# Performance work log

Hardware: AMD Instinct MI355X
Metric: run time of the kernel (lower is better)

## Reference

```python
import jax, jax.numpy as jnp
import numpy as np

EMB_DIM = 1024
N_HEADS = 16
HEAD_DIM = EMB_DIM // N_HEADS


def setup_inputs() -> dict:
    key = jax.random.key(0)
    ks = jax.random.split(key, 6)
    B, T, C = 2, 2048, EMB_DIM
    s = 1.0 / np.sqrt(C)
    return {
        "x": jax.random.normal(ks[0], (B, T, C), dtype=jnp.float32),
        "W_query": jax.random.normal(ks[1], (C, C), dtype=jnp.float32) * s,
        "W_key": jax.random.normal(ks[2], (C, C), dtype=jnp.float32) * s,
        "W_value": jax.random.normal(ks[3], (C, C), dtype=jnp.float32) * s,
        "W_out": jax.random.normal(ks[4], (C, C), dtype=jnp.float32) * s,
        "b_out": jax.random.normal(ks[5], (C,), dtype=jnp.float32) * 0.01,
    }


def reference(x, W_query, W_key, W_value, W_out, b_out):
    # x: [B, T, C]. Linear weights stored as [in, out] (transposed torch layout).
    B, T, C = x.shape
    H, D = N_HEADS, HEAD_DIM

    def split_heads(t):  # [B,T,C] -> [B,H,T,D]
        return t.reshape(B, T, H, D).transpose(0, 2, 1, 3)

    q = split_heads(x @ W_query)
    k = split_heads(x @ W_key)
    v = split_heads(x @ W_value)

    scale = 1.0 / jnp.sqrt(jnp.asarray(D, dtype=x.dtype))
    att = jnp.einsum("bhqd,bhkd->bhqk", q, k) * scale  # [B,H,T,T]
    causal = jnp.tril(jnp.ones((T, T), dtype=bool))
    att = jnp.where(causal[None, None], att, jnp.asarray(-jnp.inf, dtype=att.dtype))
    att = jax.nn.softmax(att, axis=-1)
    # dropout is identity in eval / drop_rate=0
    y = jnp.einsum("bhqk,bhkd->bhqd", att, v)  # [B,H,T,D]
    y = y.transpose(0, 2, 1, 3).reshape(B, T, C)
    return y @ W_out + b_out
```

## Files before the change

kernel.cpp:

```cpp
#include <hip/hip_runtime.h>
#include <hip/hip_bf16.h>
#include <math.h>

#define Bsz 2
#define Tsz 2048
#define Csz 1024
#define Hsz 16
#define Dsz 64

typedef __attribute__((ext_vector_type(8))) short frag8;
typedef __attribute__((ext_vector_type(4))) float f4;
typedef __attribute__((ext_vector_type(8))) unsigned short us8;
typedef __attribute__((ext_vector_type(4))) _Float16 frag4h;
typedef __attribute__((ext_vector_type(8))) _Float16 frag8h;

static __device__ __forceinline__ unsigned short f2bf(float f) {
  union { __hip_bfloat16 h; unsigned short u; } c;
  c.h = __float2bfloat16(f);
  return c.u;
}
static __device__ __forceinline__ unsigned short f2h(float f) {
  union { _Float16 h; unsigned short u; } c;
  c.h = (_Float16)f;
  return c.u;
}

#define GLDS16(g, l)                                                        \
  __builtin_amdgcn_global_load_lds(                                         \
      (const __attribute__((address_space(1))) void*)(g),                   \
      (__attribute__((address_space(3))) void*)(l), 16, 0, 0)

#define QSCALE 0.18033688f

__global__ __launch_bounds__(256) void cast_x(const float* __restrict__ x,
                                              unsigned short* __restrict__ xb) {
  const int i = (blockIdx.x * 256 + threadIdx.x) * 8;
  const float4 a = *(const float4*)(x + i);
  const float4 b = *(const float4*)(x + i + 4);
  us8 v;
  v[0] = f2bf(a.x); v[1] = f2bf(a.y); v[2] = f2bf(a.z); v[3] = f2bf(a.w);
  v[4] = f2bf(b.x); v[5] = f2bf(b.y); v[6] = f2bf(b.z); v[7] = f2bf(b.w);
  *(us8*)(xb + i) = v;
}

__global__ __launch_bounds__(256) void transpose_cast(
    const float* __restrict__ s0, const float* __restrict__ s1,
    const float* __restrict__ s2, const float* __restrict__ s3,
    unsigned short* __restrict__ d0, unsigned short* __restrict__ d1,
    unsigned short* __restrict__ d2, unsigned short* __restrict__ d3) {
  __shared__ float Ls[64][65];
  const int mat = blockIdx.x >> 8;
  const int tile = blockIdx.x & 255;
  const float* src = mat == 0 ? s0 : mat == 1 ? s1 : mat == 2 ? s2 : s3;
  unsigned short* dst = mat == 0 ? d0 : mat == 1 ? d1 : mat == 2 ? d2 : d3;
  const int tr0 = (tile >> 4) << 6, tc0 = (tile & 15) << 6;
  const int t = threadIdx.x;
  const int lr = t >> 4, lc = (t & 15) << 2;
#pragma unroll
  for (int j = 0; j < 4; ++j) {
    const float4 v = *(const float4*)(src + (size_t)(tr0 + lr + j * 16) * 1024 + tc0 + lc);
    Ls[lr + j * 16][lc + 0] = v.x;
    Ls[lr + j * 16][lc + 1] = v.y;
    Ls[lr + j * 16][lc + 2] = v.z;
    Ls[lr + j * 16][lc + 3] = v.w;
  }
  __syncthreads();
#pragma unroll
  for (int j = 0; j < 4; ++j) {
    ushort4 v;
    v.x = f2bf(Ls[lc + 0][lr + j * 16]);
    v.y = f2bf(Ls[lc + 1][lr + j * 16]);
    v.z = f2bf(Ls[lc + 2][lr + j * 16]);
    v.w = f2bf(Ls[lc + 3][lr + j * 16]);
    *(ushort4*)(dst + (size_t)(tc0 + lr + j * 16) * 1024 + tr0 + lc) = v;
  }
}

template <int MODE, int MT>
__global__ __launch_bounds__(256) void mm_bt(
    const unsigned short* __restrict__ A, const unsigned short* __restrict__ Bt,
    const float* __restrict__ bias, unsigned short* __restrict__ O0,
    unsigned short* __restrict__ O1, unsigned short* __restrict__ O2,
    float* __restrict__ Of) {
  __shared__ __align__(16) unsigned short As[MT * 32 * 64];
  __shared__ __align__(16) unsigned short Bs[128 * 64];
  const int K = 1024;
  const int tid = threadIdx.x;
  const int wave = tid >> 6, lane = tid & 63;
  const int quad = lane >> 4, l16 = lane & 15;
  const int wrow = (wave >> 1) * (MT * 16), wn = wave & 1;
  const int row0 = blockIdx.y * (MT * 32), col0 = blockIdx.x << 7;

  const int sr = lane >> 3, sg = lane & 7;
  const int g0 = sg ^ sr;
  const unsigned short* gA = A + (size_t)(row0 + wave * (MT * 8) + sr) * K + (g0 << 3);
  const unsigned short* gB = Bt + (size_t)(col0 + wave * 32 + sr) * K + (g0 << 3);

  f4 acc[MT][4];
#pragma unroll
  for (int i = 0; i < MT; ++i)
#pragma unroll
    for (int j = 0; j < 4; ++j) acc[i][j] = (f4){0.f, 0.f, 0.f, 0.f};

  for (int kk = 0; kk < K; kk += 64) {
    __syncthreads();
#pragma unroll
    for (int s = 0; s < MT; ++s)
      GLDS16(gA + kk + (size_t)(s * 8) * K, &As[(wave * (MT * 8) + s * 8) * 64]);
#pragma unroll
    for (int s = 0; s < 4; ++s)
      GLDS16(gB + kk + (size_t)(s * 8) * K, &Bs[(wave * 32 + s * 8) * 64]);
    __syncthreads();

#pragma unroll
    for (int ks = 0; ks < 2; ++ks) {
      frag8 af[MT], bf[4];
#pragma unroll
      for (int mt = 0; mt < MT; ++mt) {
        const int r = wrow + mt * 16 + l16;
        af[mt] = *(const frag8*)&As[r * 64 + (((ks * 4 + quad) ^ (l16 & 7)) << 3)];
      }
#pragma unroll
      for (int nt = 0; nt < 4; ++nt) {
        const int n = wn * 64 + nt * 16 + l16;
        bf[nt] = *(const frag8*)&Bs[n * 64 + (((ks * 4 + quad) ^ (l16 & 7)) << 3)];
      }
#pragma unroll
      for (int mt = 0; mt < MT; ++mt)
#pragma unroll
        for (int nt = 0; nt < 4; ++nt)
          acc[mt][nt] = __builtin_amdgcn_mfma_f32_16x16x32_bf16(af[mt], bf[nt], acc[mt][nt], 0, 0, 0);
    }
  }

  if (MODE == 0) {
    if (col0 < 2048) {
      const bool isK = (col0 >= 1024);
      unsigned short* dst = isK ? O1 : O0;
      const float sc = isK ? 1.0f : QSCALE;
#pragma unroll
      for (int mt = 0; mt < MT; ++mt)
#pragma unroll
        for (int nt = 0; nt < 4; ++nt) {
          const int m = row0 + wrow + mt * 16 + quad * 4;
          const int n = (col0 & 1023) + wn * 64 + nt * 16 + l16;
          const int b = m >> 11, h = n >> 6, d = n & 63;
#pragma unroll
          for (int r = 0; r < 4; ++r) {
            const int tk = (m + r) & (Tsz - 1);
            dst[(((size_t)b * Hsz + h) * Tsz + tk) * Dsz + d] = f2bf(acc[mt][nt][r] * sc);
          }
        }
    } else {
#pragma unroll
      for (int mt = 0; mt < MT; ++mt)
#pragma unroll
        for (int nt = 0; nt < 4; ++nt) {
          const int tok = row0 + wrow + mt * 16 + quad * 4;
          const int ch = (col0 - 2048) + wn * 64 + nt * 16 + l16;
          const int b = tok >> 11, tk = tok & (Tsz - 1);
          const int h = ch >> 6, d = ch & 63;
          const int t5 = tk & 31;
          const int pos = (tk & ~31) + ((t5 >> 4) << 2) + (((t5 >> 2) & 3) << 3) + (t5 & 3);
          ushort4 v;
          v.x = f2h(acc[mt][nt][0]); v.y = f2h(acc[mt][nt][1]);
          v.z = f2h(acc[mt][nt][2]); v.w = f2h(acc[mt][nt][3]);
          *(ushort4*)&O2[(((size_t)b * Hsz + h) * Dsz + d) * Tsz + pos] = v;
        }
    }
  } else {
#pragma unroll
    for (int mt = 0; mt < MT; ++mt)
#pragma unroll
      for (int nt = 0; nt < 4; ++nt) {
        const int m = row0 + wrow + mt * 16 + quad * 4;
        const int n = col0 + wn * 64 + nt * 16 + l16;
        const float bv = bias[n];
#pragma unroll
        for (int r = 0; r < 4; ++r)
          Of[(size_t)(m + r) * Csz + n] = acc[mt][nt][r] + bv;
      }
  }
}

__global__ __launch_bounds__(256, 1) void attn_mfma(
    const unsigned short* __restrict__ Qb,
    const unsigned short* __restrict__ Kb,
    const unsigned short* __restrict__ VTb,
    unsigned short* __restrict__ Y) {
  __shared__ __align__(16) unsigned short Ks[2][2048];
  __shared__ __align__(16) unsigned short Vs[2][2048];

  const int tid = threadIdx.x;
  const int wave = tid >> 6, lane = tid & 63;
  const int quad = lane >> 4, l16 = lane & 15;

  const int bh = blockIdx.x & 31;
  const int jg = blockIdx.x >> 5;
  const int ja = 4 * jg + wave;
  const int jb = 63 - ja;
  const int qa = ja << 5, qb = jb << 5;

  const unsigned short* Qh = Qb + (size_t)bh * Tsz * Dsz;
  const unsigned short* Kh = Kb + (size_t)bh * Tsz * Dsz;
  const unsigned short* Vh = VTb + (size_t)bh * Dsz * Tsz;

  const int kkey = tid >> 3, kc = tid & 7;
  const int vd = tid >> 2, vc = tid & 3;
  const unsigned short* gK = Kh + (size_t)kkey * Dsz + ((kc ^ (kkey & 7)) << 3);
  const unsigned short* gV = Vh + (size_t)vd * Tsz + ((vc ^ ((vd + (vd >> 2)) & 3)) << 3);

  frag8 qfa[2][2], qfb[2][2];
#pragma unroll
  for (int m = 0; m < 2; ++m)
#pragma unroll
    for (int ks = 0; ks < 2; ++ks) {
      qfa[m][ks] = *(const frag8*)(Qh + (size_t)(qa + m * 16 + l16) * Dsz + ks * 32 + quad * 8);
      qfb[m][ks] = *(const frag8*)(Qh + (size_t)(qb + m * 16 + l16) * Dsz + ks * 32 + quad * 8);
    }

  f4 oa[2][4], ob[2][4];
  float lsa[2] = {0.f, 0.f}, lsb[2] = {0.f, 0.f};
#pragma unroll
  for (int m = 0; m < 2; ++m)
#pragma unroll
    for (int nt = 0; nt < 4; ++nt) {
      oa[m][nt] = (f4){0.f, 0.f, 0.f, 0.f};
      ob[m][nt] = (f4){0.f, 0.f, 0.f, 0.f};
    }
  const f4 zf = (f4){0.f, 0.f, 0.f, 0.f};
  const int fl = (l16 + (l16 >> 2)) & 3;

  const int nch = 64 - 4 * jg;

  GLDS16(gK, &Ks[0][wave * 512]);
  GLDS16(gV, &Vs[0][wave * 512]);
  GLDS16(gK + (size_t)32 * Dsz, &Ks[1][wave * 512]);
  GLDS16(gV + 32, &Vs[1][wave * 512]);
  __syncthreads();

  for (int i = 0; i < nch; ++i) {
    const int bsel = i & 1;
    if (i <= jb) {
      frag8 kf[2][2];
#pragma unroll
      for (int n = 0; n < 2; ++n)
#pragma unroll
        for (int ks = 0; ks < 2; ++ks)
          kf[n][ks] = *(const frag8*)&Ks[bsel][(n * 16 + l16) * 64 + (((ks * 4 + quad) ^ (l16 & 7)) << 3)];
      frag8h vf[4];
#pragma unroll
      for (int nt = 0; nt < 4; ++nt)
        vf[nt] = *(const frag8h*)&Vs[bsel][(nt * 16 + l16) * 32 + ((quad ^ fl) << 3)];

      {
        f4 st[2][2];
#pragma unroll
        for (int n = 0; n < 2; ++n)
#pragma unroll
          for (int m = 0; m < 2; ++m) {
            f4 a = __builtin_amdgcn_mfma_f32_16x16x32_bf16(kf[n][0], qfb[m][0], zf, 0, 0, 0);
            st[n][m] = __builtin_amdgcn_mfma_f32_16x16x32_bf16(kf[n][1], qfb[m][1], a, 0, 0, 0);
          }
        const bool dm = (i == jb);
        frag4h paf[2][2];
#pragma unroll
        for (int m = 0; m < 2; ++m) {
          const int qq = m * 16 + l16;
#pragma unroll
          for (int n = 0; n < 2; ++n) {
            const int key0 = n * 16 + quad * 4;
            float p[4];
#pragma unroll
            for (int r = 0; r < 4; ++r) {
              float sv = st[n][m][r];
              if (dm && (key0 + r > qq)) sv = -INFINITY;
              p[r] = __builtin_amdgcn_exp2f(sv);
            }
            lsb[m] += (p[0] + p[1]) + (p[2] + p[3]);
            frag4h ph;
            ph[0] = (_Float16)p[0]; ph[1] = (_Float16)p[1];
            ph[2] = (_Float16)p[2]; ph[3] = (_Float16)p[3];
            paf[m][n] = ph;
          }
        }
#pragma unroll
        for (int m = 0; m < 2; ++m)
#pragma unroll
          for (int nt = 0; nt < 4; ++nt) {
            const frag4h vlo = __builtin_shufflevector(vf[nt], vf[nt], 0, 1, 2, 3);
            const frag4h vhi = __builtin_shufflevector(vf[nt], vf[nt], 4, 5, 6, 7);
            f4 a = __builtin_amdgcn_mfma_f32_16x16x16f16(paf[m][0], vlo, ob[m][nt], 0, 0, 0);
            ob[m][nt] = __builtin_amdgcn_mfma_f32_16x16x16f16(paf[m][1], vhi, a, 0, 0, 0);
          }
      }

      if (i <= ja) {
        f4 st[2][2];
#pragma unroll
        for (int n = 0; n < 2; ++n)
#pragma unroll
          for (int m = 0; m < 2; ++m) {
            f4 a = __builtin_amdgcn_mfma_f32_16x16x32_bf16(kf[n][0], qfa[m][0], zf, 0, 0, 0);
            st[n][m] = __builtin_amdgcn_mfma_f32_16x16x32_bf16(kf[n][1], qfa[m][1], a, 0, 0, 0);
          }
        const bool dm = (i == ja);
        frag4h paf[2][2];
#pragma unroll
        for (int m = 0; m < 2; ++m) {
          const int qq = m * 16 + l16;
#pragma unroll
          for (int n = 0; n < 2; ++n) {
            const int key0 = n * 16 + quad * 4;
            float p[4];
#pragma unroll
            for (int r = 0; r < 4; ++r) {
              float sv = st[n][m][r];
              if (dm && (key0 + r > qq)) sv = -INFINITY;
              p[r] = __builtin_amdgcn_exp2f(sv);
            }
            lsa[m] += (p[0] + p[1]) + (p[2] + p[3]);
            frag4h ph;
            ph[0] = (_Float16)p[0]; ph[1] = (_Float16)p[1];
            ph[2] = (_Float16)p[2]; ph[3] = (_Float16)p[3];
            paf[m][n] = ph;
          }
        }
#pragma unroll
        for (int m = 0; m < 2; ++m)
#pragma unroll
          for (int nt = 0; nt < 4; ++nt) {
            const frag4h vlo = __builtin_shufflevector(vf[nt], vf[nt], 0, 1, 2, 3);
            const frag4h vhi = __builtin_shufflevector(vf[nt], vf[nt], 4, 5, 6, 7);
            f4 a = __builtin_amdgcn_mfma_f32_16x16x16f16(paf[m][0], vlo, oa[m][nt], 0, 0, 0);
            oa[m][nt] = __builtin_amdgcn_mfma_f32_16x16x16f16(paf[m][1], vhi, a, 0, 0, 0);
          }
      }
    }
    __syncthreads();
    if (i + 2 < nch) {
      GLDS16(gK + (size_t)((i + 2) << 5) * Dsz, &Ks[bsel][wave * 512]);
      GLDS16(gV + ((i + 2) << 5), &Vs[bsel][wave * 512]);
    }
  }

#pragma unroll
  for (int m = 0; m < 2; ++m) {
    lsa[m] += __shfl_xor(lsa[m], 16);
    lsa[m] += __shfl_xor(lsa[m], 32);
    lsb[m] += __shfl_xor(lsb[m], 16);
    lsb[m] += __shfl_xor(lsb[m], 32);
  }

  const int b = bh >> 4, h = bh & 15;
#pragma unroll
  for (int m = 0; m < 2; ++m)
#pragma unroll
    for (int r = 0; r < 4; ++r) {
      const float inva = 1.f / __shfl(lsa[m], quad * 4 + r);
      const float invb = 1.f / __shfl(lsb[m], quad * 4 + r);
      const int ta = qa + m * 16 + quad * 4 + r;
      const int tb = qb + m * 16 + quad * 4 + r;
      unsigned short* ypa = Y + ((size_t)b * Tsz + ta) * Csz + h * 64 + l16;
      unsigned short* ypb = Y + ((size_t)b * Tsz + tb) * Csz + h * 64 + l16;
#pragma unroll
      for (int nt = 0; nt < 4; ++nt) {
        ypa[nt * 16] = f2bf(oa[m][nt][r] * inva);
        ypb[nt * 16] = f2bf(ob[m][nt][r] * invb);
      }
    }
}

extern "C" void kernel_launch(void* const* d_in, const int* in_sizes, int n_in,
                              void* d_out, int out_size, void* d_ws, size_t ws_size,
                              hipStream_t stream) {
  const float* x  = (const float*)d_in[0];
  const float* Wq = (const float*)d_in[1];
  const float* Wk = (const float*)d_in[2];
  const float* Wv = (const float*)d_in[3];
  const float* Wo = (const float*)d_in[4];
  const float* bo = (const float*)d_in[5];

  const size_t NEL = (size_t)Bsz * Tsz * Csz;
  const size_t WSZ = (size_t)Csz * Csz;
  unsigned short* xb  = (unsigned short*)d_ws;
  unsigned short* WT  = xb + NEL;
  unsigned short* WoT = WT + 3 * WSZ;
  unsigned short* Qb  = WoT + WSZ;
  unsigned short* Kb  = Qb + NEL;
  unsigned short* VTb = Kb + NEL;
  unsigned short* Yb  = VTb + NEL;

  cast_x<<<NEL / 2048, 256, 0, stream>>>(x, xb);
  transpose_cast<<<1024, 256, 0, stream>>>(Wq, Wk, Wv, Wo,
                                           WT, WT + WSZ, WT + 2 * WSZ, WoT);

  mm_bt<0, 4><<<dim3(24, 32), 256, 0, stream>>>(xb, WT, nullptr, Qb, Kb, VTb, nullptr);

  attn_mfma<<<256, 256, 0, stream>>>(Qb, Kb, VTb, Yb);

  mm_bt<2, 2><<<dim3(8, 64), 256, 0, stream>>>(Yb, WoT, bo, nullptr, nullptr, nullptr,
                                               (float*)d_out);
}
```

Before: 195.5 us.

## Split attention key range across four wave-pairs and reduce partials in LDS

The attention kernel now launches 512 blocks of 512 threads. Each block has four wave-pair groups, and each group handles every fourth key chunk for the same pair of query tiles. Because the softmax carries no running max, the partial output accumulators and row sums can simply be added. The first group combines them through a shared-memory buffer before normalizing and writing. This is meant to raise the wave count per CU and shorten the serial key loop of the previous one-block-per-CU launch. The cost is a 64KB LDS footprint, extra barriers and the final LDS reduction.

```diff
diff --git a/kernel.cpp b/kernel.cpp
--- a/kernel.cpp
+++ b/kernel.cpp
@@ -183,21 +183,25 @@
   }
 }
 
-__global__ __launch_bounds__(256, 1) void attn_mfma(
+__global__ __launch_bounds__(512, 4) void attn_mfma(
     const unsigned short* __restrict__ Qb,
     const unsigned short* __restrict__ Kb,
     const unsigned short* __restrict__ VTb,
     unsigned short* __restrict__ Y) {
-  __shared__ __align__(16) unsigned short Ks[2][2048];
-  __shared__ __align__(16) unsigned short Vs[2][2048];
+  __shared__ __align__(16) unsigned char SMEM[65536];
+#define KSP(spp, bb) ((unsigned short*)(SMEM + (spp) * 16384 + (bb) * 4096))
+#define VSP(spp, bb) ((unsigned short*)(SMEM + (spp) * 16384 + 8192 + (bb) * 4096))
 
   const int tid = threadIdx.x;
   const int wave = tid >> 6, lane = tid & 63;
   const int quad = lane >> 4, l16 = lane & 15;
+  const int ww = wave & 1;
+  const int sp = wave >> 1;
+  const int ltid = tid & 127;
 
   const int bh = blockIdx.x & 31;
   const int jg = blockIdx.x >> 5;
-  const int ja = 4 * jg + wave;
+  const int ja = 2 * jg + ww;
   const int jb = 63 - ja;
   const int qa = ja << 5, qb = jb << 5;
 
@@ -205,10 +209,16 @@
   const unsigned short* Kh = Kb + (size_t)bh * Tsz * Dsz;
   const unsigned short* Vh = VTb + (size_t)bh * Dsz * Tsz;
 
-  const int kkey = tid >> 3, kc = tid & 7;
-  const int vd = tid >> 2, vc = tid & 3;
-  const unsigned short* gK = Kh + (size_t)kkey * Dsz + ((kc ^ (kkey & 7)) << 3);
-  const unsigned short* gV = Vh + (size_t)vd * Tsz + ((vc ^ ((vd + (vd >> 2)) & 3)) << 3);
+  const int ke0 = ltid, ke1 = ltid + 128;
+  const int kkey0 = ke0 >> 3, kc0 = ke0 & 7;
+  const int kkey1 = ke1 >> 3, kc1 = ke1 & 7;
+  const unsigned short* gK0 = Kh + (size_t)kkey0 * Dsz + ((kc0 ^ (kkey0 & 7)) << 3);
+  const unsigned short* gK1 = Kh + (size_t)kkey1 * Dsz + ((kc1 ^ (kkey1 & 7)) << 3);
+  const int vd0 = ltid >> 2, vc0 = ltid & 3;
+  const int vd1 = vd0 + 32;
+  const unsigned short* gV0 = Vh + (size_t)vd0 * Tsz + ((vc0 ^ ((vd0 + (vd0 >> 2)) & 3)) << 3);
+  const unsigned short* gV1 = Vh + (size_t)vd1 * Tsz + ((vc0 ^ ((vd1 + (vd1 >> 2)) & 3)) << 3);
+  const int wo = ww * 512;
 
   frag8 qfa[2][2], qfb[2][2];
 #pragma unroll
@@ -231,27 +241,39 @@
   const f4 zf = (f4){0.f, 0.f, 0.f, 0.f};
   const int fl = (l16 + (l16 >> 2)) & 3;
 
-  const int nch = 64 - 4 * jg;
-
-  GLDS16(gK, &Ks[0][wave * 512]);
-  GLDS16(gV, &Vs[0][wave * 512]);
-  GLDS16(gK + (size_t)32 * Dsz, &Ks[1][wave * 512]);
-  GLDS16(gV + 32, &Vs[1][wave * 512]);
+  const int jbmax = 63 - 2 * jg;
+  const int nch = (jbmax >> 2) + 1;
+
+  {
+    const size_t kof0 = (size_t)(sp << 5) * Dsz, kof1 = (size_t)((sp + 4) << 5) * Dsz;
+    const int vof0 = sp << 5, vof1 = (sp + 4) << 5;
+    GLDS16(gK0 + kof0, KSP(sp, 0) + wo);
+    GLDS16(gK1 + kof0, KSP(sp, 0) + wo + 1024);
+    GLDS16(gV0 + vof0, VSP(sp, 0) + wo);
+    GLDS16(gV1 + vof0, VSP(sp, 0) + wo + 1024);
+    GLDS16(gK0 + kof1, KSP(sp, 1) + wo);
+    GLDS16(gK1 + kof1, KSP(sp, 1) + wo + 1024);
+    GLDS16(gV0 + vof1, VSP(sp, 1) + wo);
+    GLDS16(gV1 + vof1, VSP(sp, 1) + wo + 1024);
+  }
   __syncthreads();
 
   for (int i = 0; i < nch; ++i) {
+    const int c = sp + 4 * i;
     const int bsel = i & 1;
-    if (i <= jb) {
+    if (c <= jb) {
+      const unsigned short* Kl = KSP(sp, bsel);
+      const unsigned short* Vl = VSP(sp, bsel);
       frag8 kf[2][2];
 #pragma unroll
       for (int n = 0; n < 2; ++n)
 #pragma unroll
         for (int ks = 0; ks < 2; ++ks)
-          kf[n][ks] = *(const frag8*)&Ks[bsel][(n * 16 + l16) * 64 + (((ks * 4 + quad) ^ (l16 & 7)) << 3)];
+          kf[n][ks] = *(const frag8*)&Kl[(n * 16 + l16) * 64 + (((ks * 4 + quad) ^ (l16 & 7)) << 3)];
       frag8h vf[4];
 #pragma unroll
       for (int nt = 0; nt < 4; ++nt)
-        vf[nt] = *(const frag8h*)&Vs[bsel][(nt * 16 + l16) * 32 + ((quad ^ fl) << 3)];
+        vf[nt] = *(const frag8h*)&Vl[(nt * 16 + l16) * 32 + ((quad ^ fl) << 3)];
 
       {
         f4 st[2][2];
@@ -262,7 +284,7 @@
             f4 a = __builtin_amdgcn_mfma_f32_16x16x32_bf16(kf[n][0], qfb[m][0], zf, 0, 0, 0);
             st[n][m] = __builtin_amdgcn_mfma_f32_16x16x32_bf16(kf[n][1], qfb[m][1], a, 0, 0, 0);
           }
-        const bool dm = (i == jb);
+        const bool dm = (c == jb);
         frag4h paf[2][2];
 #pragma unroll
         for (int m = 0; m < 2; ++m) {
@@ -295,7 +317,7 @@
           }
       }
 
-      if (i <= ja) {
+      if (c <= ja) {
         f4 st[2][2];
 #pragma unroll
         for (int n = 0; n < 2; ++n)
@@ -304,7 +326,7 @@
             f4 a = __builtin_amdgcn_mfma_f32_16x16x32_bf16(kf[n][0], qfa[m][0], zf, 0, 0, 0);
             st[n][m] = __builtin_amdgcn_mfma_f32_16x16x32_bf16(kf[n][1], qfa[m][1], a, 0, 0, 0);
           }
-        const bool dm = (i == ja);
+        const bool dm = (c == ja);
         frag4h paf[2][2];
 #pragma unroll
         for (int m = 0; m < 2; ++m) {
@@ -339,36 +361,90 @@
     }
     __syncthreads();
     if (i + 2 < nch) {
-      GLDS16(gK + (size_t)((i + 2) << 5) * Dsz, &Ks[bsel][wave * 512]);
-      GLDS16(gV + ((i + 2) << 5), &Vs[bsel][wave * 512]);
-    }
-  }
-
-#pragma unroll
-  for (int m = 0; m < 2; ++m) {
-    lsa[m] += __shfl_xor(lsa[m], 16);
-    lsa[m] += __shfl_xor(lsa[m], 32);
-    lsb[m] += __shfl_xor(lsb[m], 16);
-    lsb[m] += __shfl_xor(lsb[m], 32);
-  }
-
-  const int b = bh >> 4, h = bh & 15;
-#pragma unroll
-  for (int m = 0; m < 2; ++m)
-#pragma unroll
-    for (int r = 0; r < 4; ++r) {
-      const float inva = 1.f / __shfl(lsa[m], quad * 4 + r);
-      const float invb = 1.f / __shfl(lsb[m], quad * 4 + r);
-      const int ta = qa + m * 16 + quad * 4 + r;
-      const int tb = qb + m * 16 + quad * 4 + r;
-      unsigned short* ypa = Y + ((size_t)b * Tsz + ta) * Csz + h * 64 + l16;
-      unsigned short* ypb = Y + ((size_t)b * Tsz + tb) * Csz + h * 64 + l16;
-#pragma unroll
-      for (int nt = 0; nt < 4; ++nt) {
-        ypa[nt * 16] = f2bf(oa[m][nt][r] * inva);
-        ypb[nt * 16] = f2bf(ob[m][nt][r] * invb);
-      }
-    }
+      const int c2 = sp + 4 * (i + 2);
+      const size_t kof = (size_t)(c2 << 5) * Dsz;
+      const int vof = c2 << 5;
+      GLDS16(gK0 + kof, KSP(sp, bsel) + wo);
+      GLDS16(gK1 + kof, KSP(sp, bsel) + wo + 1024);
+      GLDS16(gV0 + vof, VSP(sp, bsel) + wo);
+      GLDS16(gV1 + vof, VSP(sp, bsel) + wo + 1024);
+    }
+  }
+
+  float* comb = (float*)SMEM;
+  const int slot = (sp - 1) * 2 + ww;
+  float* cp = comb + (size_t)(slot * 64 + lane) * 36;
+
+  if (sp != 0) {
+#pragma unroll
+    for (int m = 0; m < 2; ++m)
+#pragma unroll
+      for (int nt = 0; nt < 4; ++nt)
+        *(f4*)(cp + m * 16 + nt * 4) = ob[m][nt];
+    cp[32] = lsb[0]; cp[33] = lsb[1];
+  }
+  __syncthreads();
+  if (sp == 0) {
+#pragma unroll
+    for (int s = 0; s < 3; ++s) {
+      const float* rp = comb + (size_t)((s * 2 + ww) * 64 + lane) * 36;
+#pragma unroll
+      for (int m = 0; m < 2; ++m)
+#pragma unroll
+        for (int nt = 0; nt < 4; ++nt)
+          ob[m][nt] += *(const f4*)(rp + m * 16 + nt * 4);
+      lsb[0] += rp[32]; lsb[1] += rp[33];
+    }
+  }
+  __syncthreads();
+  if (sp != 0) {
+#pragma unroll
+    for (int m = 0; m < 2; ++m)
+#pragma unroll
+      for (int nt = 0; nt < 4; ++nt)
+        *(f4*)(cp + m * 16 + nt * 4) = oa[m][nt];
+    cp[32] = lsa[0]; cp[33] = lsa[1];
+  }
+  __syncthreads();
+  if (sp == 0) {
+#pragma unroll
+    for (int s = 0; s < 3; ++s) {
+      const float* rp = comb + (size_t)((s * 2 + ww) * 64 + lane) * 36;
+#pragma unroll
+      for (int m = 0; m < 2; ++m)
+#pragma unroll
+        for (int nt = 0; nt < 4; ++nt)
+          oa[m][nt] += *(const f4*)(rp + m * 16 + nt * 4);
+      lsa[0] += rp[32]; lsa[1] += rp[33];
+    }
+
+#pragma unroll
+    for (int m = 0; m < 2; ++m) {
+      lsa[m] += __shfl_xor(lsa[m], 16);
+      lsa[m] += __shfl_xor(lsa[m], 32);
+      lsb[m] += __shfl_xor(lsb[m], 16);
+      lsb[m] += __shfl_xor(lsb[m], 32);
+    }
+    const int b = bh >> 4, h = bh & 15;
+#pragma unroll
+    for (int m = 0; m < 2; ++m)
+#pragma unroll
+      for (int r = 0; r < 4; ++r) {
+        const float inva = 1.f / __shfl(lsa[m], quad * 4 + r);
+        const float invb = 1.f / __shfl(lsb[m], quad * 4 + r);
+        const int ta = qa + m * 16 + quad * 4 + r;
+        const int tb = qb + m * 16 + quad * 4 + r;
+        unsigned short* ypa = Y + ((size_t)b * Tsz + ta) * Csz + h * 64 + l16;
+        unsigned short* ypb = Y + ((size_t)b * Tsz + tb) * Csz + h * 64 + l16;
+#pragma unroll
+        for (int nt = 0; nt < 4; ++nt) {
+          ypa[nt * 16] = f2bf(oa[m][nt][r] * inva);
+          ypb[nt * 16] = f2bf(ob[m][nt][r] * invb);
+        }
+      }
+  }
+#undef KSP
+#undef VSP
 }
 
 extern "C" void kernel_launch(void* const* d_in, const int* in_sizes, int n_in,
@@ -397,7 +473,7 @@
 
   mm_bt<0, 4><<<dim3(24, 32), 256, 0, stream>>>(xb, WT, nullptr, Qb, Kb, VTb, nullptr);
 
-  attn_mfma<<<256, 256, 0, stream>>>(Qb, Kb, VTb, Yb);
+  attn_mfma<<<512, 512, 0, stream>>>(Qb, Kb, VTb, Yb);
 
   mm_bt<2, 2><<<dim3(8, 64), 256, 0, stream>>>(Yb, WoT, bo, nullptr, nullptr, nullptr,
                                                (float*)d_out);
```

Measured after the change: 266.5 us. +36.3%, slower.
